# Kernel tuning notes

Measured on AMD Instinct MI355X. Metric: run time of the kernel, lower is better.

The kernel has to match this reference:

```python
import jax, jax.numpy as jnp
import numpy as np

GROUPS = 8
N_HEADS = 8
EPS = 1e-5


def setup_inputs() -> dict:
    key = jax.random.key(0)
    ks = jax.random.split(key, 3)
    B, C, H, W = 8, 512, 32, 32
    x = jax.random.normal(ks[0], (B, C, H, W), dtype=jnp.float32)
    # Conv2d(C, 3C, 1) weight squeezed to [3C, C]; kaiming-ish scale
    qkv_w = jax.random.normal(ks[1], (3 * C, C), dtype=jnp.float32) * (1.0 / np.sqrt(C))
    proj_w = jax.random.normal(ks[2], (C, C), dtype=jnp.float32) * (1.0 / np.sqrt(C))
    return {
        "x": x,
        "norm_gamma": jnp.ones((C,), jnp.float32),
        "norm_beta": jnp.zeros((C,), jnp.float32),
        "qkv_w": qkv_w,
        "qkv_b": jnp.zeros((3 * C,), jnp.float32),
        "proj_w": proj_w,
        "proj_b": jnp.zeros((C,), jnp.float32),
    }


def reference(x, norm_gamma, norm_beta, qkv_w, qkv_b, proj_w, proj_b):
    B, C, H, W = x.shape
    nh = N_HEADS
    hd = C // nh
    scale = hd ** (-0.5)
    S = H * W

    # GroupNorm(8, C): normalize over (C/G, H, W) within each group
    xg = x.reshape(B, GROUPS, -1)
    mean = xg.mean(axis=-1, keepdims=True)
    var = xg.var(axis=-1, keepdims=True)
    xn = ((xg - mean) * jax.lax.rsqrt(var + EPS)).reshape(B, C, H, W)
    xn = xn * norm_gamma[None, :, None, None] + norm_beta[None, :, None, None]

    # 1x1 conv QKV == per-pixel matmul
    qkv = jnp.einsum('oc,bchw->bohw', qkv_w, xn) + qkv_b[None, :, None, None]
    qkv = qkv.reshape(B, 3, nh, hd, S)
    q, k, v = qkv[:, 0], qkv[:, 1], qkv[:, 2]  # each (B, nh, hd, S)

    # attn[b,h,s,t] = sum_d q[b,h,d,s] k[b,h,d,t] * scale
    attn = jax.nn.softmax(jnp.einsum('bhds,bhdt->bhst', q, k) * scale, axis=-1)
    out = jnp.einsum('bhst,bhdt->bhds', attn, v).reshape(B, C, H, W)

    # 1x1 conv projection + residual
    return x + jnp.einsum('oc,bchw->bohw', proj_w, out) + proj_b[None, :, None, None]
```

## Files before the change

### kernel.cpp

```cpp
#include <hip/hip_runtime.h>
#include <hip/hip_bf16.h>

typedef __attribute__((ext_vector_type(4))) float  f32x4;
typedef __attribute__((ext_vector_type(8))) _Float16 f16x8;
typedef __attribute__((ext_vector_type(4))) _Float16 f16x4;
typedef __attribute__((ext_vector_type(4))) float  float4v;
typedef __attribute__((ext_vector_type(4))) unsigned int uint4v;

#define BATCH   8
#define CDIM    512
#define SLEN    1024
#define NHEADS  8
#define HDIM    64
#define QSCALE  0.1803368801111f
#define FIXED_M 8.0f


__device__ __forceinline__ f32x4 mfma16x16x16f16(f16x4 a, f16x4 b, f32x4 c){
#if __has_builtin(__builtin_amdgcn_mfma_f32_16x16x16f16)
    return __builtin_amdgcn_mfma_f32_16x16x16f16(a, b, c, 0, 0, 0);
#else
    asm volatile("v_mfma_f32_16x16x16_f16 %0, %1, %2, %0"
                 : "+v"(c) : "v"(a), "v"(b));
    return c;
#endif
}

__device__ __forceinline__ float fast_exp2(float x){
    float r;
    asm("v_exp_f32 %0, %1" : "=v"(r) : "v"(x));
    return r;
}

__device__ __forceinline__ void stage16(const void* g, void* l, int lane){
#if __has_builtin(__builtin_amdgcn_global_load_lds)
    __builtin_amdgcn_global_load_lds((const __attribute__((address_space(1))) void*)g,
                                     (__attribute__((address_space(3))) void*)l, 16, 0, 0);
#else
    *(f16x8*)((char*)l + lane * 16) = *(const f16x8*)g;
#endif
}


__global__ __launch_bounds__(256) void prep(
    const float4v* __restrict__ qkvw, f16x4* __restrict__ wq,
    const float4v* __restrict__ projw, f16x4* __restrict__ pw,
    const float* __restrict__ x, float* __restrict__ part)
{
    __shared__ float s1[256], s2[256];
    if (blockIdx.x < 1024){
        int i = blockIdx.x * 256 + threadIdx.x;
        if (i < 196608){
            float4v v = qkvw[i];
            wq[i] = (f16x4){ (_Float16)v[0], (_Float16)v[1], (_Float16)v[2], (_Float16)v[3] };
        } else {
            int j = i - 196608;
            float4v v = projw[j];
            pw[j] = (f16x4){ (_Float16)v[0], (_Float16)v[1], (_Float16)v[2], (_Float16)v[3] };
        }
        return;
    }
    int bid = blockIdx.x - 1024;
    int bg = bid >> 3, pc = bid & 7;
    const float4v* xp = (const float4v*)(x + (size_t)bg * 65536 + (size_t)pc * 8192);
    float sum = 0.f, sq = 0.f;
    for (int i = threadIdx.x; i < 2048; i += 256){
        float4v v = xp[i];
        sum += (v[0] + v[1]) + (v[2] + v[3]);
        sq  += (v[0]*v[0] + v[1]*v[1]) + (v[2]*v[2] + v[3]*v[3]);
    }
    s1[threadIdx.x] = sum; s2[threadIdx.x] = sq;
    __syncthreads();
    for (int o = 128; o > 0; o >>= 1){
        if (threadIdx.x < o){ s1[threadIdx.x] += s1[threadIdx.x + o];
                              s2[threadIdx.x] += s2[threadIdx.x + o]; }
        __syncthreads();
    }
    if (threadIdx.x == 0){
        part[bid * 2 + 0] = s1[0];
        part[bid * 2 + 1] = s2[0];
    }
}


__global__ __launch_bounds__(256) void gn_apply(
    const float* __restrict__ x, const float* __restrict__ part,
    const float* __restrict__ gamma, const float* __restrict__ beta,
    _Float16* __restrict__ xnT)
{
    int b = blockIdx.z, g = blockIdx.y, s0 = blockIdx.x * 64;
    int bg = b * 8 + g, c0 = g * 64;

    float sum = 0.f, sq = 0.f;
#pragma unroll
    for (int p = 0; p < 8; p++){
        sum += part[bg * 16 + p * 2 + 0];
        sq  += part[bg * 16 + p * 2 + 1];
    }
    float mean = sum * (1.f / 65536.f);
    float var  = sq  * (1.f / 65536.f) - mean * mean;
    float inv  = rsqrtf(var + 1e-5f);

    __shared__ _Float16 tile[64 * 66];

    int tx = threadIdx.x & 15, ty = threadIdx.x >> 4;
#pragma unroll
    for (int j = 0; j < 4; j++){
        int c = ty + 16 * j;
        float ga = gamma[c0 + c] * inv;
        float be = beta[c0 + c] - mean * ga;
        float4v v = *(const float4v*)(x + ((size_t)(b * CDIM + c0 + c)) * SLEN + s0 + tx * 4);
#pragma unroll
        for (int i = 0; i < 4; i++)
            tile[(tx * 4 + i) * 66 + c] = (_Float16)(v[i] * ga + be);
    }
    __syncthreads();

    int s = threadIdx.x >> 2, cq = (threadIdx.x & 3) * 16;
    const unsigned int* lsrc = (const unsigned int*)((const unsigned short*)tile + s * 66 + cq);
    uint4v lo = { lsrc[0], lsrc[1], lsrc[2], lsrc[3] };
    uint4v hi = { lsrc[4], lsrc[5], lsrc[6], lsrc[7] };
    unsigned int* dst = (unsigned int*)(xnT + ((size_t)b * SLEN + s0 + s) * CDIM + c0 + cq);
    *(uint4v*)dst       = lo;
    *(uint4v*)(dst + 4) = hi;
}


#define GEMM_CORE(APTR, BPTR)                                                   \
    __shared__ __align__(16) char smem[32768];                                  \
    int tid = threadIdx.x;                                                      \
    int wid = tid >> 6, lane = tid & 63;                                        \
    int w0 = wid >> 1, w1 = wid & 1;                                            \
    int lr = lane & 15, lg = lane >> 4;                                         \
    int slotg = ((lane & 3) ^ ((lane >> 3) & 3)) * 16;                          \
    int srow = lane >> 2;                                                       \
    const char* agp = (const char*)(APTR) +                                     \
        ((size_t)(bo + wid * 32 + srow) * CDIM) * 2 + slotg;                    \
    const char* bgp = (const char*)(BPTR) +                                     \
        ((size_t)(sgbase + wid * 32 + srow) * CDIM) * 2 + slotg;                \
    char* lA = smem + wid * 2048;                                               \
    char* lB = smem + 8192 + wid * 2048;                                        \
    f32x4 acc[4][4];                                                            \
    _Pragma("unroll") for (int i = 0; i < 4; i++)                               \
    _Pragma("unroll") for (int j = 0; j < 4; j++)                               \
        acc[i][j] = (f32x4){0.f, 0.f, 0.f, 0.f};                                \
    _Pragma("unroll") for (int j = 0; j < 2; j++){                              \
        stage16(agp + j * 16384, lA + j * 1024, lane);                          \
        stage16(bgp + j * 16384, lB + j * 1024, lane);                          \
    }                                                                           \
    __syncthreads();                                                            \
    int xt = ((lr >> 1) & 3) << 4;                                              \
    for (int it = 0; it < 16; ++it){                                            \
        int cur = (it & 1) * 16384;                                             \
        if (it + 1 < 16){                                                       \
            int nxt = 16384 - cur, ko = (it + 1) * 64;                          \
            _Pragma("unroll") for (int j = 0; j < 2; j++){                      \
                stage16(agp + j * 16384 + ko, lA + nxt + j * 1024, lane);       \
                stage16(bgp + j * 16384 + ko, lB + nxt + j * 1024, lane);       \
            }                                                                   \
        }                                                                       \
        const char* Ac = smem + cur + (w0 * 64 + lr) * 64;                      \
        const char* Bc = smem + cur + 8192 + (w1 * 64 + lr) * 64;               \
        f16x8 af[4], bfr[4];                                                    \
        _Pragma("unroll") for (int t = 0; t < 4; t++){                          \
            af[t]  = *(const f16x8*)(Ac + t * 1024 + ((lg * 16) ^ xt));         \
            bfr[t] = *(const f16x8*)(Bc + t * 1024 + ((lg * 16) ^ xt));         \
        }                                                                       \
        _Pragma("unroll") for (int i = 0; i < 4; i++)                           \
        _Pragma("unroll") for (int j = 0; j < 4; j++)                           \
            acc[i][j] = __builtin_amdgcn_mfma_f32_16x16x32_f16(af[i], bfr[j],   \
                                                               acc[i][j], 0, 0, 0); \
        __syncthreads();                                                        \
    }


__global__ __launch_bounds__(256) void qkv_gemm(
    const _Float16* __restrict__ wq, const _Float16* __restrict__ xnT,
    const float* __restrict__ qkvb,
    _Float16* __restrict__ qT, _Float16* __restrict__ kT, _Float16* __restrict__ vv)
{
    int b  = blockIdx.z;
    int bo = blockIdx.y * 128;
    size_t sgbase = (size_t)b * SLEN + blockIdx.x * 128;

    GEMM_CORE(wq, xnT)

    int obase = bo + w0 * 64, sbase = blockIdx.x * 128 + w1 * 64;
    int p = obase >> 9;
    int h = (obase >> 6) & 7;
    size_t bh = (size_t)b * NHEADS + h;

    if (p == 2){
#pragma unroll
        for (int i = 0; i < 4; i++){
            int d0 = i * 16 + lg * 4;
            float4v bias = *(const float4v*)(qkvb + obase + d0);
#pragma unroll
            for (int j = 0; j < 4; j++){
                int s = sbase + j * 16 + lr;
                _Float16* vp2 = vv + (bh * HDIM) * SLEN + s;
                vp2[(size_t)(d0 + 0) * SLEN] = (_Float16)(acc[i][j][0] + bias[0]);
                vp2[(size_t)(d0 + 1) * SLEN] = (_Float16)(acc[i][j][1] + bias[1]);
                vp2[(size_t)(d0 + 2) * SLEN] = (_Float16)(acc[i][j][2] + bias[2]);
                vp2[(size_t)(d0 + 3) * SLEN] = (_Float16)(acc[i][j][3] + bias[3]);
            }
        }
    } else {
        float sc = (p == 0) ? QSCALE : 1.f;
        char* wreg = smem + wid * 8192;
#pragma unroll
        for (int i = 0; i < 4; i++){
            int d0 = i * 16 + lg * 4;
            float4v bias = *(const float4v*)(qkvb + obase + d0);
            int slotbase = (2 * i + (lg >> 1)) * 16;
            int inoff = (lg & 1) * 8;
#pragma unroll
            for (int j = 0; j < 4; j++){
                int s_loc = j * 16 + lr;
                f16x4 pk = { (_Float16)((acc[i][j][0] + bias[0]) * sc),
                             (_Float16)((acc[i][j][1] + bias[1]) * sc),
                             (_Float16)((acc[i][j][2] + bias[2]) * sc),
                             (_Float16)((acc[i][j][3] + bias[3]) * sc) };
                *(f16x4*)(wreg + s_loc * 128 + (slotbase ^ ((s_loc & 7) << 4)) + inoff) = pk;
            }
        }
        _Float16* dst = (p == 0 ? qT : kT) + (bh * SLEN + sbase) * HDIM;
#pragma unroll
        for (int m = 0; m < 8; m++){
            int s_loc = m * 8 + (lane >> 3);
            f16x8 row = *(const f16x8*)(wreg + s_loc * 128 + (((lane & 7) ^ (s_loc & 7)) << 4));
            *(f16x8*)(dst + (size_t)s_loc * HDIM + (lane & 7) * 8) = row;
        }
    }
}


__global__ __launch_bounds__(256) void proj_gemm(
    const _Float16* __restrict__ pw, const _Float16* __restrict__ outT,
    const float* __restrict__ pb, const float* __restrict__ x,
    float* __restrict__ y)
{
    int b  = blockIdx.z;
    int bo = blockIdx.y * 128;
    size_t sgbase = (size_t)b * SLEN + blockIdx.x * 128;

    GEMM_CORE(pw, outT)

    int obase = bo + w0 * 64, sbase = blockIdx.x * 128 + w1 * 64;

#pragma unroll
    for (int i = 0; i < 4; i++){
        int o0 = obase + i * 16 + lg * 4;
        float4v bias = *(const float4v*)(pb + o0);
#pragma unroll
        for (int j = 0; j < 4; j++){
            int s = sbase + j * 16 + lr;
#pragma unroll
            for (int r = 0; r < 4; r++){
                size_t idx = ((size_t)b * CDIM + o0 + r) * SLEN + s;
                y[idx] = acc[i][j][r] + bias[r] + x[idx];
            }
        }
    }
}


#define ATTN_CHUNK(c)                                                           \
    {                                                                           \
        const char* kbuf = smem + ((c) & 3) * 16384;                            \
        const char* vbuf = kbuf + 8192;                                         \
        f16x8 kf[4][2];                                                         \
        _Pragma("unroll") for (int i = 0; i < 4; i++){                          \
            const char* kr = kbuf + (16 * i + lr) * 128;                        \
            kf[i][0] = *(const f16x8*)(kr + ((lg * 16) ^ r7));                  \
            kf[i][1] = *(const f16x8*)(kr + ((64 + lg * 16) ^ r7));             \
        }                                                                       \
        f16x4 vf[4][4];                                                         \
        _Pragma("unroll") for (int i = 0; i < 4; i++)                           \
        _Pragma("unroll") for (int dt = 0; dt < 4; dt++)                        \
            vf[i][dt] = *(const f16x4*)(vbuf + (dt * 16 + lr) * 128             \
                                        + ((32 * i + 8 * lg) ^ r7));            \
        _Pragma("unroll") for (int sj = 0; sj < 2; sj++){                       \
            f32x4 st[4];                                                        \
            _Pragma("unroll") for (int i = 0; i < 4; i++){                      \
                f32x4 z = (f32x4){-FIXED_M, -FIXED_M, -FIXED_M, -FIXED_M};      \
                z = __builtin_amdgcn_mfma_f32_16x16x32_f16(kf[i][0], qf[sj][0], z, 0, 0, 0); \
                z = __builtin_amdgcn_mfma_f32_16x16x32_f16(kf[i][1], qf[sj][1], z, 0, 0, 0); \
                st[i] = z;                                                      \
            }                                                                   \
            f16x4 pb[4];                                                        \
            _Pragma("unroll") for (int i = 0; i < 4; i++){                      \
                float p0 = fast_exp2(st[i][0]);                                 \
                float p1 = fast_exp2(st[i][1]);                                 \
                float p2 = fast_exp2(st[i][2]);                                 \
                float p3 = fast_exp2(st[i][3]);                                 \
                pb[i] = (f16x4){ (_Float16)p0, (_Float16)p1,                    \
                                 (_Float16)p2, (_Float16)p3 };                  \
            }                                                                   \
            _Pragma("unroll") for (int i = 0; i < 4; i++)                       \
                osum[sj] = mfma16x16x16f16(ones, pb[i], osum[sj]);              \
            _Pragma("unroll") for (int dt = 0; dt < 4; dt++){                   \
                f32x4 o = oac[dt][sj];                                          \
                _Pragma("unroll") for (int i = 0; i < 4; i++)                   \
                    o = mfma16x16x16f16(vf[i][dt], pb[i], o);                   \
                oac[dt][sj] = o;                                                \
            }                                                                   \
        }                                                                       \
    }

__global__ __launch_bounds__(256) void attn_kernel(
    const _Float16* __restrict__ qT, const _Float16* __restrict__ kT,
    const _Float16* __restrict__ vv, _Float16* __restrict__ outT)
{
    __shared__ __align__(16) char smem[65536];

    int id = blockIdx.x;
    int h = id & 7, rr = id >> 3;
    int sx = rr & 7, b = rr >> 3;
    size_t bh = (size_t)b * NHEADS + h;
    int tid = threadIdx.x;
    int wid = tid >> 6, lane = tid & 63;
    int lr = lane & 15, lg = lane >> 4;
    int sbase = sx * 128 + wid * 32;

    const _Float16* qp = qT + bh * SLEN * HDIM;
    const _Float16* kp = kT + bh * SLEN * HDIM;
    const _Float16* vp = vv + bh * HDIM * SLEN;

    int r8 = lane >> 3;
    int srow = wid * 16 + r8;
    int scol = ((lane & 7) * 16) ^ ((srow & 7) << 4);
    const char* kg = (const char*)kp + (size_t)srow * 128  + scol;
    const char* vg = (const char*)vp + (size_t)srow * 2048 + scol;
    char* kd = smem + wid * 2048;
    char* vd = smem + 8192 + wid * 2048;

    f16x8 qf[2][2];
#pragma unroll
    for (int sj = 0; sj < 2; sj++)
#pragma unroll
        for (int kk = 0; kk < 2; kk++)
            qf[sj][kk] = *(const f16x8*)(qp + (size_t)(sbase + sj * 16 + lr) * HDIM + kk * 32 + lg * 8);

    f32x4 oac[4][2], osum[2];
#pragma unroll
    for (int dt = 0; dt < 4; dt++){
        oac[dt][0] = (f32x4){0.f, 0.f, 0.f, 0.f};
        oac[dt][1] = (f32x4){0.f, 0.f, 0.f, 0.f};
    }
    osum[0] = (f32x4){0.f, 0.f, 0.f, 0.f};
    osum[1] = (f32x4){0.f, 0.f, 0.f, 0.f};
    const f16x4 ones = { (_Float16)1.f, (_Float16)1.f, (_Float16)1.f, (_Float16)1.f };

#pragma unroll
    for (int c = 0; c < 2; c++){
        stage16(kg + (size_t)c * 8192,         kd + c * 16384,        lane);
        stage16(kg + (size_t)c * 8192 + 1024,  kd + c * 16384 + 1024, lane);
        stage16(vg + (size_t)c * 128,          vd + c * 16384,        lane);
        stage16(vg + (size_t)c * 128 + 16384,  vd + c * 16384 + 1024, lane);
    }
    __syncthreads();

    int r7 = (lr & 7) << 4;

    for (int c0 = 0; c0 < 16; c0 += 2){
        if (c0 + 2 < 16){
#pragma unroll
            for (int u = 2; u < 4; u++){
                int c = c0 + u, bb = (c & 3) * 16384;
                stage16(kg + (size_t)c * 8192,         kd + bb,        lane);
                stage16(kg + (size_t)c * 8192 + 1024,  kd + bb + 1024, lane);
                stage16(vg + (size_t)c * 128,          vd + bb,        lane);
                stage16(vg + (size_t)c * 128 + 16384,  vd + bb + 1024, lane);
            }
        }
        ATTN_CHUNK(c0)
        ATTN_CHUNK(c0 + 1)
        __syncthreads();
    }

#pragma unroll
    for (int sj = 0; sj < 2; sj++){
        float inv = 1.f / osum[sj][0];
        int s = sbase + sj * 16 + lr;
#pragma unroll
        for (int dt = 0; dt < 4; dt++){
            f16x4 ob = { (_Float16)(oac[dt][sj][0] * inv), (_Float16)(oac[dt][sj][1] * inv),
                         (_Float16)(oac[dt][sj][2] * inv), (_Float16)(oac[dt][sj][3] * inv) };
            *(f16x4*)(outT + ((size_t)b * SLEN + s) * CDIM + h * HDIM + dt * 16 + lg * 4) = ob;
        }
    }
}


extern "C" void kernel_launch(void* const* d_in, const int* in_sizes, int n_in,
                              void* d_out, int out_size, void* d_ws, size_t ws_size,
                              hipStream_t stream)
{
    const float* x     = (const float*)d_in[0];
    const float* gamma = (const float*)d_in[1];
    const float* beta  = (const float*)d_in[2];
    const float* qkvw  = (const float*)d_in[3];
    const float* qkvb  = (const float*)d_in[4];
    const float* projw = (const float*)d_in[5];
    const float* projb = (const float*)d_in[6];
    float* out = (float*)d_out;

    char* ws = (char*)d_ws;
    _Float16* wq_bf = (_Float16*)(ws);
    _Float16* pw_bf = (_Float16*)(ws + 1572864);
    _Float16* xnT   = (_Float16*)(ws + 2097152);
    _Float16* qT    = (_Float16*)(ws + 2097152 + 8388608);
    _Float16* kT    = (_Float16*)(ws + 2097152 + 16777216);
    _Float16* vv    = (_Float16*)(ws + 2097152 + 25165824);
    _Float16* outT  = (_Float16*)(ws + 2097152 + 33554432);
    float*    part  = (float*)(ws + 2097152 + 33554432);

    prep<<<1536, 256, 0, stream>>>((const float4v*)qkvw, (f16x4*)wq_bf,
                                   (const float4v*)projw, (f16x4*)pw_bf, x, part);
    gn_apply<<<dim3(16, 8, 8), 256, 0, stream>>>(x, part, gamma, beta, xnT);
    qkv_gemm<<<dim3(8, 12, 8), 256, 0, stream>>>(wq_bf, xnT, qkvb, qT, kT, vv);
    attn_kernel<<<512, 256, 0, stream>>>(qT, kT, vv, outT);
    proj_gemm<<<dim3(8, 4, 8), 256, 0, stream>>>(pw_bf, outT, projb, x, out);
}
```

Measured before the change: 82.85 us.

## Transpose proj epilogue through LDS for coalesced stores; stagger attention KV chunk order

The projection GEMM epilogue now writes bias-added accumulators to per-wave LDS scratch and reads them back transposed, so each lane loads the residual and stores the output as float4 runs along the spatial dimension instead of scattered scalar accesses. Shared memory grows slightly to hold the padded scratch. In the attention kernel, each query-block group starts its K/V chunk walk at a different offset so concurrent blocks for the same head read different chunks at any moment, spreading cache and channel traffic. The added LDS round trip and the larger LDS footprint could reduce occupancy.

```diff
diff --git a/kernel.cpp b/kernel.cpp
--- a/kernel.cpp
+++ b/kernel.cpp
@@ -127,7 +127,7 @@
 
 
 #define GEMM_CORE(APTR, BPTR)                                                   \
-    __shared__ __align__(16) char smem[32768];                                  \
+    __shared__ __align__(16) char smem[34816];                                  \
     int tid = threadIdx.x;                                                      \
     int wid = tid >> 6, lane = tid & 63;                                        \
     int w0 = wid >> 1, w1 = wid & 1;                                            \
@@ -247,19 +247,37 @@
     GEMM_CORE(pw, outT)
 
     int obase = bo + w0 * 64, sbase = blockIdx.x * 128 + w1 * 64;
-
-#pragma unroll
-    for (int i = 0; i < 4; i++){
-        int o0 = obase + i * 16 + lg * 4;
-        float4v bias = *(const float4v*)(pb + o0);
-#pragma unroll
-        for (int j = 0; j < 4; j++){
-            int s = sbase + j * 16 + lr;
-#pragma unroll
-            for (int r = 0; r < 4; r++){
-                size_t idx = ((size_t)b * CDIM + o0 + r) * SLEN + s;
-                y[idx] = acc[i][j][r] + bias[r] + x[idx];
+    float* wreg = (float*)(smem + wid * 8704);
+
+#pragma unroll
+    for (int half = 0; half < 2; half++){
+        asm volatile("" ::: "memory");
+#pragma unroll
+        for (int jj = 0; jj < 2; jj++){
+            int j = half * 2 + jj;
+            int srow2 = jj * 16 + lr;
+#pragma unroll
+            for (int i = 0; i < 4; i++){
+                int c0 = i * 16 + lg * 4;
+                float4v bias = *(const float4v*)(pb + obase + c0);
+                float4v v = { acc[i][j][0] + bias[0], acc[i][j][1] + bias[1],
+                              acc[i][j][2] + bias[2], acc[i][j][3] + bias[3] };
+                *(float4v*)(wreg + srow2 * 68 + c0) = v;
             }
+        }
+        asm volatile("" ::: "memory");
+        int cl = lane >> 3, sq = (lane & 7) * 4;
+#pragma unroll
+        for (int g = 0; g < 8; g++){
+            int c = cl + 8 * g;
+            float r0 = wreg[(sq + 0) * 68 + c];
+            float r1 = wreg[(sq + 1) * 68 + c];
+            float r2 = wreg[(sq + 2) * 68 + c];
+            float r3 = wreg[(sq + 3) * 68 + c];
+            size_t idx = ((size_t)b * CDIM + obase + c) * SLEN + sbase + half * 32 + sq;
+            float4v xr = *(const float4v*)(x + idx);
+            float4v o = { r0 + xr[0], r1 + xr[1], r2 + xr[2], r3 + xr[3] };
+            *(float4v*)(y + idx) = o;
         }
     }
 }
@@ -322,6 +340,7 @@
     int wid = tid >> 6, lane = tid & 63;
     int lr = lane & 15, lg = lane >> 4;
     int sbase = sx * 128 + wid * 32;
+    int phase = sx << 1;
 
     const _Float16* qp = qT + bh * SLEN * HDIM;
     const _Float16* kp = kT + bh * SLEN * HDIM;
@@ -354,28 +373,29 @@
 
 #pragma unroll
     for (int c = 0; c < 2; c++){
-        stage16(kg + (size_t)c * 8192,         kd + c * 16384,        lane);
-        stage16(kg + (size_t)c * 8192 + 1024,  kd + c * 16384 + 1024, lane);
-        stage16(vg + (size_t)c * 128,          vd + c * 16384,        lane);
-        stage16(vg + (size_t)c * 128 + 16384,  vd + c * 16384 + 1024, lane);
+        int pc = (c + phase) & 15;
+        stage16(kg + (size_t)pc * 8192,         kd + c * 16384,        lane);
+        stage16(kg + (size_t)pc * 8192 + 1024,  kd + c * 16384 + 1024, lane);
+        stage16(vg + (size_t)pc * 128,          vd + c * 16384,        lane);
+        stage16(vg + (size_t)pc * 128 + 16384,  vd + c * 16384 + 1024, lane);
     }
     __syncthreads();
 
     int r7 = (lr & 7) << 4;
 
-    for (int c0 = 0; c0 < 16; c0 += 2){
-        if (c0 + 2 < 16){
+    for (int cc0 = 0; cc0 < 16; cc0 += 2){
+        if (cc0 + 2 < 16){
 #pragma unroll
             for (int u = 2; u < 4; u++){
-                int c = c0 + u, bb = (c & 3) * 16384;
-                stage16(kg + (size_t)c * 8192,         kd + bb,        lane);
-                stage16(kg + (size_t)c * 8192 + 1024,  kd + bb + 1024, lane);
-                stage16(vg + (size_t)c * 128,          vd + bb,        lane);
-                stage16(vg + (size_t)c * 128 + 16384,  vd + bb + 1024, lane);
+                int lc = cc0 + u, pc = (lc + phase) & 15, bb = (lc & 3) * 16384;
+                stage16(kg + (size_t)pc * 8192,         kd + bb,        lane);
+                stage16(kg + (size_t)pc * 8192 + 1024,  kd + bb + 1024, lane);
+                stage16(vg + (size_t)pc * 128,          vd + bb,        lane);
+                stage16(vg + (size_t)pc * 128 + 16384,  vd + bb + 1024, lane);
             }
         }
-        ATTN_CHUNK(c0)
-        ATTN_CHUNK(c0 + 1)
+        ATTN_CHUNK(cc0)
+        ATTN_CHUNK(cc0 + 1)
         __syncthreads();
     }
 
```

Result: faster. 79.40 us (-4.2%).
